# Optimization experiments

Hardware: AMD Instinct MI355X
Metric: run time of the kernel (lower is better)

Reference implementation:

```python
import jax, jax.numpy as jnp
import numpy as np

_SAMPLING_EPS = 1e-5


def setup_inputs() -> dict:
    key = jax.random.key(0)
    k1, k2, k3, k4, k5, k6 = jax.random.split(key, 6)
    B, V = 128, 128000
    return {
        "logits": jax.random.normal(k1, (B, V), dtype=jnp.float32),
        "temperature": jax.random.uniform(k2, (B,), dtype=jnp.float32),
        "min_p": jax.random.uniform(k3, (B,), dtype=jnp.float32),
        "top_k": jax.random.randint(k4, (B,), 0, 1024),
        "top_p": jax.random.uniform(k5, (B,), dtype=jnp.float32),
        "q": jax.random.uniform(k6, (B, V), dtype=jnp.float32),
        "num_logprobs": 20,
    }


def reference(logits, temperature, min_p, top_k, top_p, q, num_logprobs):
    B, V = logits.shape
    # raw logprobs computed BEFORE any processing (as in Sampler.forward)
    raw_logprobs = jax.nn.log_softmax(logits, axis=-1)
    # greedy sample on unscaled logits
    greedy = jnp.argmax(logits, axis=-1)
    # temperature scaling
    lt = logits / temperature[:, None]
    # min-p filtering
    probs = jax.nn.softmax(lt, axis=-1)
    max_p = jnp.max(probs, axis=-1, keepdims=True)
    lt = jnp.where(probs >= min_p[:, None] * max_p, lt, -jnp.inf)
    # top-k / top-p filtering on ascending-sorted logits (vLLM style)
    idx = jnp.argsort(lt, axis=-1)                       # ascending
    ls = jnp.take_along_axis(lt, idx, axis=-1)
    k = jnp.clip(top_k, 1, V)
    kth = jnp.take_along_axis(ls, (V - k)[:, None], axis=-1)  # k-th largest value
    ls = jnp.where(ls < kth, -jnp.inf, ls)
    ps = jax.nn.softmax(ls, axis=-1)
    csum = jnp.cumsum(ps, axis=-1)
    pmask = csum <= (1.0 - top_p)[:, None]
    pmask = pmask.at[:, -1].set(False)                   # always keep the max token
    ls = jnp.where(pmask, -jnp.inf, ls)
    inv = jnp.argsort(idx, axis=-1)                      # inverse permutation (scatter back)
    filtered = jnp.take_along_axis(ls, inv, axis=-1)
    # exponential-race sampling: argmax(probs / Exp(1)) ~ Categorical(probs)
    probs2 = jax.nn.softmax(filtered, axis=-1)
    expo = -jnp.log(jnp.clip(q, 1e-10, 1.0))
    rand_sampled = jnp.argmax(probs2 / expo, axis=-1)
    sampled = jnp.where(temperature < _SAMPLING_EPS, greedy, rand_sampled)
    # gather_logprobs: top-k logprobs + sampled-token logprob + rank
    topk_lp, topk_idx = jax.lax.top_k(raw_logprobs, num_logprobs)
    tok_lp = jnp.take_along_axis(raw_logprobs, sampled[:, None], axis=-1)  # (B,1)
    ranks = jnp.sum(raw_logprobs >= tok_lp, axis=-1)
    out_idx = jnp.concatenate([sampled[:, None], topk_idx], axis=1).astype(jnp.int32)
    out_lp = jnp.concatenate([tok_lp, topk_lp], axis=1)  # (B, num_logprobs+1)
    return (sampled[:, None].astype(jnp.int32), out_idx, out_lp, ranks)
```

## Files before the change

### kernel.cpp

```cpp
#include <hip/hip_runtime.h>
#include <math.h>

#define S_CHUNKS 16
#define NB 1024
#define C_CAP 2048
#define BLKA 256
#define BLK2 512
#define LCAP 1024
#define LCAP2 512
#define FLOORB 682
#define BIN_SCALE ((float)NB / 12.0f)

__device__ __forceinline__ int bin_of(float x) {
  int b = (int)floorf((x + 6.0f) * BIN_SCALE);
  return min(max(b, 0), NB - 1);
}
__device__ __forceinline__ unsigned long long pack_vi(float v, int idx) {
  return ((unsigned long long)__float_as_uint(v) << 32) | (unsigned int)idx;
}
__device__ __forceinline__ unsigned long long okey(float v, int idx) {
  unsigned int u = __float_as_uint(v);
  u = (u & 0x80000000u) ? ~u : (u | 0x80000000u);
  return ((unsigned long long)u << 32) | (unsigned long long)(0x7fffffffu - (unsigned int)idx);
}
__device__ __forceinline__ float okey_val(unsigned long long k) {
  unsigned int hi = (unsigned int)(k >> 32);
  unsigned int u = (hi & 0x80000000u) ? (hi & 0x7fffffffu) : ~hi;
  return __uint_as_float(u);
}
__device__ __forceinline__ int okey_idx(unsigned long long k) {
  return (int)(0x7fffffffu - (unsigned int)k);
}

__global__ __launch_bounds__(BLKA)
void kA_hist(const float* __restrict__ logits, int V, int chunkElems,
             unsigned short* __restrict__ chist, float* __restrict__ psum,
             unsigned long long* __restrict__ plist, int* __restrict__ pcnt) {
  const int row = blockIdx.y, chunk = blockIdx.x, tid = threadIdx.x;
  const float* lrow = logits + (size_t)row * V;
  const int start = chunk * chunkElems;
  const int end = min(start + chunkElems, V);
  __shared__ unsigned int hist[NB];
  __shared__ unsigned long long lst[LCAP2];
  __shared__ float rs[BLKA];
  __shared__ int lcnt;
  for (int i = tid; i < NB; i += BLKA) hist[i] = 0u;
  if (tid == 0) lcnt = 0;
  __syncthreads();
  float sum = 0.0f;
  const int n = max(end - start, 0);
  const int n4 = n >> 2;
  const float4* p4 = (const float4*)(lrow + start);
  for (int i = tid; i < n4; i += BLKA) {
    float4 a = p4[i];
    float va[4] = {a.x, a.y, a.z, a.w};
    #pragma unroll
    for (int c = 0; c < 4; c++) {
      float x = va[c];
      int b = bin_of(x);
      atomicAdd(&hist[b], 1u);
      sum += __expf(fminf(x, 70.0f) - 6.0f);
      if (b >= FLOORB) {
        int p = atomicAdd(&lcnt, 1);
        if (p < LCAP2) lst[p] = pack_vi(x, start + (i << 2) + c);
      }
    }
  }
  for (int j = (n4 << 2) + tid; j < n; j += BLKA) {
    float x = lrow[start + j];
    int b = bin_of(x);
    atomicAdd(&hist[b], 1u);
    sum += __expf(fminf(x, 70.0f) - 6.0f);
    if (b >= FLOORB) {
      int p = atomicAdd(&lcnt, 1);
      if (p < LCAP2) lst[p] = pack_vi(x, start + j);
    }
  }
  __syncthreads();
  rs[tid] = sum;
  __syncthreads();
  for (int s = BLKA / 2; s > 0; s >>= 1) {
    if (tid < s) rs[tid] += rs[tid + s];
    __syncthreads();
  }
  const size_t rc = (size_t)row * S_CHUNKS + chunk;
  if (tid == 0) { psum[rc] = rs[0]; pcnt[rc] = lcnt; }
  unsigned short* hrow = chist + rc * NB;
  for (int j = tid; j < NB; j += BLKA)
    hrow[j] = (unsigned short)min(hist[j], 65535u);
  int m = min(lcnt, LCAP2);
  unsigned long long* prow = plist + rc * LCAP2;
  for (int j = tid; j < m; j += BLKA) prow[j] = lst[j];
}

__global__ __launch_bounds__(BLKA)
void kB_select(const unsigned short* __restrict__ chist,
               const float* __restrict__ psum, const int* __restrict__ pcnt,
               const int* __restrict__ top_k, const int* __restrict__ nl_ptr,
               int V, int* __restrict__ bstar_out, float* __restrict__ lse_out,
               int* __restrict__ cnt, int* __restrict__ mode) {
  const int row = blockIdx.x, tid = threadIdx.x;
  __shared__ unsigned int h[NB];
  __shared__ int s_b, s_m;
  for (int i = tid; i < NB; i += BLKA) {
    unsigned int s = 0;
    for (int c = 0; c < S_CHUNKS; c++)
      s += chist[((size_t)row * S_CHUNKS + c) * NB + i];
    h[i] = s;
  }
  if (tid == 0) { s_b = 0; s_m = 0; }
  __syncthreads();
  if (tid < S_CHUNKS) atomicMax(&s_m, pcnt[(size_t)row * S_CHUNKS + tid]);
  for (int off = 1; off < NB; off <<= 1) {
    unsigned int t0[NB / BLKA];
    #pragma unroll
    for (int k = 0; k < NB / BLKA; k++) {
      int i = tid + k * BLKA;
      t0[k] = (i + off < NB) ? h[i + off] : 0u;
    }
    __syncthreads();
    #pragma unroll
    for (int k = 0; k < NB / BLKA; k++) h[tid + k * BLKA] += t0[k];
    __syncthreads();
  }
  int ke = top_k[row]; ke = min(max(ke, 1), V);
  int Kp = max(ke, nl_ptr[0]);
  #pragma unroll
  for (int k = 0; k < NB / BLKA; k++) {
    int i = tid + k * BLKA;
    if ((int)h[i] >= Kp) atomicMax(&s_b, i);
  }
  __syncthreads();
  if (tid == 0) {
    bstar_out[row] = s_b;
    float t = 0.0f;
    for (int c = 0; c < S_CHUNKS; c++) t += psum[(size_t)row * S_CHUNKS + c];
    lse_out[row] = 6.0f + logf(t);
    cnt[row] = 0;
    mode[row] = (s_b >= FLOORB && s_m <= LCAP2) ? 1 : 0;
  }
}

__global__ __launch_bounds__(BLKA)
void kC_collect(const float* __restrict__ logits, int V, int chunkElems,
                const int* __restrict__ bstar_in, const int* __restrict__ mode,
                const unsigned long long* __restrict__ plist,
                const int* __restrict__ pcnt, int* __restrict__ cnt,
                float* __restrict__ cand_val, int* __restrict__ cand_idx) {
  const int row = blockIdx.y, chunk = blockIdx.x, tid = threadIdx.x;
  const int bstar = bstar_in[row];
  __shared__ float lv[LCAP];
  __shared__ int   li[LCAP];
  __shared__ int   lcnt, gbase;
  if (tid == 0) lcnt = 0;
  __syncthreads();
  const size_t rc = (size_t)row * S_CHUNKS + chunk;
  if (mode[row]) {
    int m = min(pcnt[rc], LCAP2);
    const unsigned long long* prow = plist + rc * LCAP2;
    for (int j = tid; j < m; j += BLKA) {
      unsigned long long k = prow[j];
      float x = __uint_as_float((unsigned int)(k >> 32));
      int idx = (int)(unsigned int)k;
      if (bin_of(x) >= bstar) {
        int p = atomicAdd(&lcnt, 1);
        if (p < LCAP) { lv[p] = x; li[p] = idx; }
      }
    }
  } else {
    const float* lrow = logits + (size_t)row * V;
    const int start = chunk * chunkElems;
    const int end = min(start + chunkElems, V);
    const int n = max(end - start, 0);
    const int n4 = n >> 2;
    const float4* p4 = (const float4*)(lrow + start);
    for (int i = tid; i < n4; i += BLKA) {
      float4 a = p4[i];
      float va[4] = {a.x, a.y, a.z, a.w};
      #pragma unroll
      for (int c = 0; c < 4; c++) {
        if (bin_of(va[c]) >= bstar) {
          int p = atomicAdd(&lcnt, 1);
          if (p < LCAP) { lv[p] = va[c]; li[p] = start + (i << 2) + c; }
        }
      }
    }
    for (int j = (n4 << 2) + tid; j < n; j += BLKA) {
      float x = lrow[start + j];
      if (bin_of(x) >= bstar) {
        int p = atomicAdd(&lcnt, 1);
        if (p < LCAP) { lv[p] = x; li[p] = start + j; }
      }
    }
  }
  __syncthreads();
  int m = min(lcnt, LCAP);
  if (tid == 0) gbase = atomicAdd(&cnt[row], m);
  __syncthreads();
  int gb = gbase;
  for (int j = tid; j < m; j += BLKA) {
    int pos = gb + j;
    if (pos < C_CAP) {
      cand_val[(size_t)row * C_CAP + pos] = lv[j];
      cand_idx[(size_t)row * C_CAP + pos] = li[j];
    }
  }
}

__global__ __launch_bounds__(BLK2)
void k2_sample(const float* __restrict__ temperature,
               const float* __restrict__ min_p,
               const int* __restrict__ top_k,
               const float* __restrict__ top_p,
               const float* __restrict__ q,
               const int* __restrict__ nl_ptr,
               int V, int B,
               const float* __restrict__ cand_val,
               const int* __restrict__ cand_idx,
               const int* __restrict__ cnt_in,
               const float* __restrict__ lse_in,
               float* __restrict__ out) {
  const int row = blockIdx.x, tid = threadIdx.x;
  __shared__ int   scan[NB + 1];
  __shared__ unsigned long long bkt[C_CAP];
  __shared__ float sv[C_CAP];
  __shared__ int   si[C_CAP];
  __shared__ float ss[C_CAP];
  __shared__ float st[BLK2], rf[BLK2], rf2[BLK2];
  __shared__ int   ri[BLK2];
  __shared__ int   s_fail;

  int c = cnt_in[row]; c = min(c, C_CAP); c = max(c, 1);

  for (int i = tid; i <= NB; i += BLK2) scan[i] = 0;
  __syncthreads();

  unsigned long long mykey[4];
  int mybin[4], mya[4], myn = 0;
  #pragma unroll
  for (int r = 0; r < 4; r++) {
    int i = tid + r * BLK2;
    if (i < c) {
      float v = cand_val[(size_t)row * C_CAP + i];
      int id = cand_idx[(size_t)row * C_CAP + i];
      mykey[myn] = okey(v, id);
      int b = bin_of(v);
      mybin[myn] = b;
      mya[myn] = atomicAdd(&scan[b], 1);
      myn++;
    }
  }
  __syncthreads();
  for (int off = 1; off < NB; off <<= 1) {
    int i0 = tid, i1 = tid + BLK2;
    int t0 = (i0 + off < NB) ? scan[i0 + off] : 0;
    int t1 = (i1 + off < NB) ? scan[i1 + off] : 0;
    __syncthreads();
    scan[i0] += t0; scan[i1] += t1;
    __syncthreads();
  }
  for (int r = 0; r < myn; r++)
    bkt[scan[mybin[r] + 1] + mya[r]] = mykey[r];
  __syncthreads();
  for (int r = 0; r < myn; r++) {
    int gs = scan[mybin[r] + 1], ge = scan[mybin[r]];
    unsigned long long k0 = mykey[r];
    int rk = 0;
    for (int j = gs; j < ge; j++) if (bkt[j] > k0) rk++;
    int pos = gs + rk;
    sv[pos] = okey_val(k0);
    si[pos] = okey_idx(k0);
  }
  __syncthreads();

  float temp = temperature[row];
  bool ug = (temp < 1e-5f);
  float rt = 1.0f / (ug ? 1.0f : temp);
  float mp = min_p[row], tp = top_p[row];
  int nl = nl_ptr[0];
  int ke = top_k[row]; ke = min(max(ke, 1), V); ke = min(ke, c);
  float v0 = sv[0];
  float lt0 = v0 * rt;

  float ltk = sv[ke - 1] * rt;
  float kth = (expf(ltk - lt0) >= mp) ? ltk : -INFINITY;

  if (tid == 0) s_fail = c;
  __syncthreads();
  for (int i = tid; i < c; i += BLK2) {
    float ltj = sv[i] * rt;
    if (!((expf(ltj - lt0) >= mp) && (ltj >= kth))) { atomicMin(&s_fail, i); break; }
  }
  __syncthreads();
  int n1 = s_fail; if (n1 < 1) n1 = 1;
  __syncthreads();

  int L = (c + BLK2 - 1) / BLK2;
  int base = tid * L;
  int lim = min(base + L, c);
  float run = 0.0f;
  for (int j = base; j < lim; j++) {
    float pj = (j < n1) ? expf(sv[j] * rt - lt0) : 0.0f;
    run += pj; ss[j] = run;
  }
  st[tid] = run;
  __syncthreads();
  for (int off = 1; off < BLK2; off <<= 1) {
    float t0 = (tid >= off) ? st[tid - off] : 0.0f;
    __syncthreads();
    st[tid] += t0;
    __syncthreads();
  }
  float offv = (tid > 0) ? st[tid - 1] : 0.0f;
  for (int j = base; j < lim; j++) ss[j] += offv;
  __syncthreads();
  float Z1 = ss[n1 - 1];

  if (tid == 0) s_fail = n1;
  __syncthreads();
  for (int i = tid; i < n1; i += BLK2) {
    if (i > 0 && !((1.0f - ss[i - 1] / Z1) > (1.0f - tp))) { atomicMin(&s_fail, i); break; }
  }
  __syncthreads();
  int n2 = s_fail; if (n2 < 1) n2 = 1;
  __syncthreads();
  float Z2 = ss[n2 - 1];

  const float* qrow = q + (size_t)row * V;
  float bsc = -INFINITY; int bidx = 0x7fffffff; float bval = 0.0f;
  for (int i = tid; i < n2; i += BLK2) {
    float pj = expf(sv[i] * rt - lt0);
    float qv = qrow[si[i]];
    qv = fminf(fmaxf(qv, 1e-10f), 1.0f);
    float sc = (pj / Z2) / (-logf(qv));
    if (sc > bsc || (sc == bsc && si[i] < bidx)) { bsc = sc; bidx = si[i]; bval = sv[i]; }
  }
  rf[tid] = bsc; ri[tid] = bidx; rf2[tid] = bval;
  __syncthreads();
  for (int s = BLK2 / 2; s > 0; s >>= 1) {
    if (tid < s) {
      if (rf[tid + s] > rf[tid] ||
          (rf[tid + s] == rf[tid] && ri[tid + s] < ri[tid])) {
        rf[tid] = rf[tid + s]; ri[tid] = ri[tid + s]; rf2[tid] = rf2[tid + s];
      }
    }
    __syncthreads();
  }
  int sampled = ug ? si[0] : ri[0];
  float val_s = ug ? sv[0] : rf2[0];
  float lse = lse_in[row];
  float tok_lp = val_s - lse;
  __syncthreads();

  if (tid == 0) s_fail = c;
  __syncthreads();
  for (int i = tid; i < c; i += BLK2)
    if (!((sv[i] - lse) >= tok_lp)) { atomicMin(&s_fail, i); break; }
  __syncthreads();
  int rank = s_fail;

  int W = nl + 1;
  if (tid == 0) {
    out[row] = (float)sampled;
    out[B + row * W] = (float)sampled;
    out[B + B * W + row * W] = tok_lp;
    out[B + 2 * B * W + row] = (float)rank;
  }
  for (int t = tid; t < nl; t += BLK2) {
    out[B + row * W + 1 + t] = (float)si[t];
    out[B + B * W + row * W + 1 + t] = sv[t] - lse;
  }
}

extern "C" void kernel_launch(void* const* d_in, const int* in_sizes, int n_in,
                              void* d_out, int out_size, void* d_ws, size_t ws_size,
                              hipStream_t stream) {
  const float* logits      = (const float*)d_in[0];
  const float* temperature = (const float*)d_in[1];
  const float* min_p       = (const float*)d_in[2];
  const int*   top_k       = (const int*)d_in[3];
  const float* top_p       = (const float*)d_in[4];
  const float* q           = (const float*)d_in[5];
  const int*   nl_ptr      = (const int*)d_in[6];

  int B = in_sizes[1];
  int V = in_sizes[0] / B;
  float* out = (float*)d_out;
  int chunkElems = ((V + S_CHUNKS - 1) / S_CHUNKS + 3) & ~3;

  unsigned char* w = (unsigned char*)d_ws;
  unsigned long long* plist = (unsigned long long*)w; w += (size_t)B * S_CHUNKS * LCAP2 * sizeof(unsigned long long);
  unsigned short* chist = (unsigned short*)w;         w += (size_t)B * S_CHUNKS * NB * sizeof(unsigned short);
  float* psum = (float*)w;                            w += (size_t)B * S_CHUNKS * sizeof(float);
  int* pcnt = (int*)w;                                w += (size_t)B * S_CHUNKS * sizeof(int);
  int* bstar = (int*)w;                               w += (size_t)B * sizeof(int);
  float* lse = (float*)w;                             w += (size_t)B * sizeof(float);
  int* cnt = (int*)w;                                 w += (size_t)B * sizeof(int);
  int* mode = (int*)w;                                w += (size_t)B * sizeof(int);
  float* cand_val = (float*)w;                        w += (size_t)B * C_CAP * sizeof(float);
  int* cand_idx = (int*)w;                            w += (size_t)B * C_CAP * sizeof(int);

  hipLaunchKernelGGL(kA_hist, dim3(S_CHUNKS, B), dim3(BLKA), 0, stream,
                     logits, V, chunkElems, chist, psum, plist, pcnt);
  hipLaunchKernelGGL(kB_select, dim3(B), dim3(BLKA), 0, stream,
                     chist, psum, pcnt, top_k, nl_ptr, V, bstar, lse, cnt, mode);
  hipLaunchKernelGGL(kC_collect, dim3(S_CHUNKS, B), dim3(BLKA), 0, stream,
                     logits, V, chunkElems, bstar, mode, plist, pcnt, cnt,
                     cand_val, cand_idx);
  hipLaunchKernelGGL(k2_sample, dim3(B), dim3(BLK2), 0, stream,
                     temperature, min_p, top_k, top_p, q, nl_ptr, V, B,
                     cand_val, cand_idx, cnt, lse, out);
}
```

Before: 185.8 us.

## Fuse bin selection, candidate collection and sampling into one per-row kernel

Merges the select, collect and sample kernels into a single per-row block. The block sums the chunk histograms, finds the threshold bin, scatters candidates straight into shared-memory bucket slots using the histogram prefix offsets, and then samples. This removes two kernel launches and the global candidate buffers. The fallback path now scans the whole row with only one block per row instead of sixteen. The histogram pass also processes two float4 loads per iteration to raise memory-level parallelism.

```diff
diff --git a/kernel.cpp b/kernel.cpp
--- a/kernel.cpp
+++ b/kernel.cpp
@@ -6,7 +6,6 @@
 #define C_CAP 2048
 #define BLKA 256
 #define BLK2 512
-#define LCAP 1024
 #define LCAP2 512
 #define FLOORB 682
 #define BIN_SCALE ((float)NB / 12.0f)
@@ -51,7 +50,26 @@
   const int n = max(end - start, 0);
   const int n4 = n >> 2;
   const float4* p4 = (const float4*)(lrow + start);
-  for (int i = tid; i < n4; i += BLKA) {
+  int i = tid;
+  for (; i + BLKA < n4; i += 2 * BLKA) {
+    float4 a = p4[i], b2 = p4[i + BLKA];
+    float va[8] = {a.x, a.y, a.z, a.w, b2.x, b2.y, b2.z, b2.w};
+    int ia[8];
+    #pragma unroll
+    for (int c = 0; c < 4; c++) { ia[c] = start + (i << 2) + c; ia[c + 4] = start + ((i + BLKA) << 2) + c; }
+    #pragma unroll
+    for (int c = 0; c < 8; c++) {
+      float x = va[c];
+      int b = bin_of(x);
+      atomicAdd(&hist[b], 1u);
+      sum += __expf(fminf(x, 70.0f) - 6.0f);
+      if (b >= FLOORB) {
+        int p = atomicAdd(&lcnt, 1);
+        if (p < LCAP2) lst[p] = pack_vi(x, ia[c]);
+      }
+    }
+  }
+  for (; i < n4; i += BLKA) {
     float4 a = p4[i];
     float va[4] = {a.x, a.y, a.z, a.w};
     #pragma unroll
@@ -93,183 +111,129 @@
   for (int j = tid; j < m; j += BLKA) prow[j] = lst[j];
 }
 
-__global__ __launch_bounds__(BLKA)
-void kB_select(const unsigned short* __restrict__ chist,
-               const float* __restrict__ psum, const int* __restrict__ pcnt,
-               const int* __restrict__ top_k, const int* __restrict__ nl_ptr,
-               int V, int* __restrict__ bstar_out, float* __restrict__ lse_out,
-               int* __restrict__ cnt, int* __restrict__ mode) {
+__global__ __launch_bounds__(BLK2)
+void k2_fused(const float* __restrict__ logits,
+              const float* __restrict__ temperature,
+              const float* __restrict__ min_p,
+              const int* __restrict__ top_k,
+              const float* __restrict__ top_p,
+              const float* __restrict__ q,
+              const int* __restrict__ nl_ptr,
+              int V, int B, int chunkElems,
+              const unsigned short* __restrict__ chist,
+              const float* __restrict__ psum,
+              const unsigned long long* __restrict__ plist,
+              const int* __restrict__ pcnt,
+              float* __restrict__ out) {
   const int row = blockIdx.x, tid = threadIdx.x;
-  __shared__ unsigned int h[NB];
-  __shared__ int s_b, s_m;
-  for (int i = tid; i < NB; i += BLKA) {
-    unsigned int s = 0;
-    for (int c = 0; c < S_CHUNKS; c++)
-      s += chist[((size_t)row * S_CHUNKS + c) * NB + i];
-    h[i] = s;
-  }
-  if (tid == 0) { s_b = 0; s_m = 0; }
-  __syncthreads();
-  if (tid < S_CHUNKS) atomicMax(&s_m, pcnt[(size_t)row * S_CHUNKS + tid]);
-  for (int off = 1; off < NB; off <<= 1) {
-    unsigned int t0[NB / BLKA];
-    #pragma unroll
-    for (int k = 0; k < NB / BLKA; k++) {
-      int i = tid + k * BLKA;
-      t0[k] = (i + off < NB) ? h[i + off] : 0u;
-    }
-    __syncthreads();
-    #pragma unroll
-    for (int k = 0; k < NB / BLKA; k++) h[tid + k * BLKA] += t0[k];
-    __syncthreads();
-  }
-  int ke = top_k[row]; ke = min(max(ke, 1), V);
-  int Kp = max(ke, nl_ptr[0]);
-  #pragma unroll
-  for (int k = 0; k < NB / BLKA; k++) {
-    int i = tid + k * BLKA;
-    if ((int)h[i] >= Kp) atomicMax(&s_b, i);
-  }
-  __syncthreads();
-  if (tid == 0) {
-    bstar_out[row] = s_b;
-    float t = 0.0f;
-    for (int c = 0; c < S_CHUNKS; c++) t += psum[(size_t)row * S_CHUNKS + c];
-    lse_out[row] = 6.0f + logf(t);
-    cnt[row] = 0;
-    mode[row] = (s_b >= FLOORB && s_m <= LCAP2) ? 1 : 0;
-  }
-}
-
-__global__ __launch_bounds__(BLKA)
-void kC_collect(const float* __restrict__ logits, int V, int chunkElems,
-                const int* __restrict__ bstar_in, const int* __restrict__ mode,
-                const unsigned long long* __restrict__ plist,
-                const int* __restrict__ pcnt, int* __restrict__ cnt,
-                float* __restrict__ cand_val, int* __restrict__ cand_idx) {
-  const int row = blockIdx.y, chunk = blockIdx.x, tid = threadIdx.x;
-  const int bstar = bstar_in[row];
-  __shared__ float lv[LCAP];
-  __shared__ int   li[LCAP];
-  __shared__ int   lcnt, gbase;
-  if (tid == 0) lcnt = 0;
-  __syncthreads();
-  const size_t rc = (size_t)row * S_CHUNKS + chunk;
-  if (mode[row]) {
-    int m = min(pcnt[rc], LCAP2);
-    const unsigned long long* prow = plist + rc * LCAP2;
-    for (int j = tid; j < m; j += BLKA) {
-      unsigned long long k = prow[j];
-      float x = __uint_as_float((unsigned int)(k >> 32));
-      int idx = (int)(unsigned int)k;
-      if (bin_of(x) >= bstar) {
-        int p = atomicAdd(&lcnt, 1);
-        if (p < LCAP) { lv[p] = x; li[p] = idx; }
-      }
-    }
-  } else {
-    const float* lrow = logits + (size_t)row * V;
-    const int start = chunk * chunkElems;
-    const int end = min(start + chunkElems, V);
-    const int n = max(end - start, 0);
-    const int n4 = n >> 2;
-    const float4* p4 = (const float4*)(lrow + start);
-    for (int i = tid; i < n4; i += BLKA) {
-      float4 a = p4[i];
-      float va[4] = {a.x, a.y, a.z, a.w};
-      #pragma unroll
-      for (int c = 0; c < 4; c++) {
-        if (bin_of(va[c]) >= bstar) {
-          int p = atomicAdd(&lcnt, 1);
-          if (p < LCAP) { lv[p] = va[c]; li[p] = start + (i << 2) + c; }
-        }
-      }
-    }
-    for (int j = (n4 << 2) + tid; j < n; j += BLKA) {
-      float x = lrow[start + j];
-      if (bin_of(x) >= bstar) {
-        int p = atomicAdd(&lcnt, 1);
-        if (p < LCAP) { lv[p] = x; li[p] = start + j; }
-      }
-    }
-  }
-  __syncthreads();
-  int m = min(lcnt, LCAP);
-  if (tid == 0) gbase = atomicAdd(&cnt[row], m);
-  __syncthreads();
-  int gb = gbase;
-  for (int j = tid; j < m; j += BLKA) {
-    int pos = gb + j;
-    if (pos < C_CAP) {
-      cand_val[(size_t)row * C_CAP + pos] = lv[j];
-      cand_idx[(size_t)row * C_CAP + pos] = li[j];
-    }
-  }
-}
-
-__global__ __launch_bounds__(BLK2)
-void k2_sample(const float* __restrict__ temperature,
-               const float* __restrict__ min_p,
-               const int* __restrict__ top_k,
-               const float* __restrict__ top_p,
-               const float* __restrict__ q,
-               const int* __restrict__ nl_ptr,
-               int V, int B,
-               const float* __restrict__ cand_val,
-               const int* __restrict__ cand_idx,
-               const int* __restrict__ cnt_in,
-               const float* __restrict__ lse_in,
-               float* __restrict__ out) {
-  const int row = blockIdx.x, tid = threadIdx.x;
-  __shared__ int   scan[NB + 1];
+  __shared__ int h[NB + 1];
+  __shared__ int cur[NB];
   __shared__ unsigned long long bkt[C_CAP];
   __shared__ float sv[C_CAP];
   __shared__ int   si[C_CAP];
   __shared__ float ss[C_CAP];
   __shared__ float st[BLK2], rf[BLK2], rf2[BLK2];
   __shared__ int   ri[BLK2];
-  __shared__ int   s_fail;
-
-  int c = cnt_in[row]; c = min(c, C_CAP); c = max(c, 1);
-
-  for (int i = tid; i <= NB; i += BLK2) scan[i] = 0;
-  __syncthreads();
-
-  unsigned long long mykey[4];
-  int mybin[4], mya[4], myn = 0;
+  __shared__ int   s_fail, s_b, s_m;
+  __shared__ float s_lse;
+
   #pragma unroll
-  for (int r = 0; r < 4; r++) {
-    int i = tid + r * BLK2;
-    if (i < c) {
-      float v = cand_val[(size_t)row * C_CAP + i];
-      int id = cand_idx[(size_t)row * C_CAP + i];
-      mykey[myn] = okey(v, id);
-      int b = bin_of(v);
-      mybin[myn] = b;
-      mya[myn] = atomicAdd(&scan[b], 1);
-      myn++;
-    }
-  }
-  __syncthreads();
+  for (int k = 0; k < NB / BLK2; k++) {
+    int i = tid + k * BLK2;
+    int s = 0;
+    for (int c = 0; c < S_CHUNKS; c++)
+      s += chist[((size_t)row * S_CHUNKS + c) * NB + i];
+    h[i] = s;
+    cur[i] = 0;
+  }
+  if (tid == 0) { h[NB] = 0; s_b = 0; s_m = 0; s_fail = 0; }
+  __syncthreads();
+  if (tid < S_CHUNKS) atomicMax(&s_m, pcnt[(size_t)row * S_CHUNKS + tid]);
   for (int off = 1; off < NB; off <<= 1) {
-    int i0 = tid, i1 = tid + BLK2;
-    int t0 = (i0 + off < NB) ? scan[i0 + off] : 0;
-    int t1 = (i1 + off < NB) ? scan[i1 + off] : 0;
-    __syncthreads();
-    scan[i0] += t0; scan[i1] += t1;
-    __syncthreads();
-  }
-  for (int r = 0; r < myn; r++)
-    bkt[scan[mybin[r] + 1] + mya[r]] = mykey[r];
-  __syncthreads();
-  for (int r = 0; r < myn; r++) {
-    int gs = scan[mybin[r] + 1], ge = scan[mybin[r]];
-    unsigned long long k0 = mykey[r];
+    int t0[NB / BLK2];
+    #pragma unroll
+    for (int k = 0; k < NB / BLK2; k++) {
+      int i = tid + k * BLK2;
+      t0[k] = (i + off < NB) ? h[i + off] : 0;
+    }
+    __syncthreads();
+    #pragma unroll
+    for (int k = 0; k < NB / BLK2; k++) h[tid + k * BLK2] += t0[k];
+    __syncthreads();
+  }
+  int nl = nl_ptr[0];
+  int ke = top_k[row]; ke = min(max(ke, 1), V);
+  int Kp = max(ke, nl);
+  #pragma unroll
+  for (int k = 0; k < NB / BLK2; k++) {
+    int i = tid + k * BLK2;
+    if (h[i] >= Kp) atomicMax(&s_b, i);
+  }
+  if (tid == 0) {
+    float t = 0.0f;
+    for (int c = 0; c < S_CHUNKS; c++) t += psum[(size_t)row * S_CHUNKS + c];
+    s_lse = 6.0f + logf(t);
+  }
+  __syncthreads();
+  const int bstar = s_b;
+  const bool fast = (bstar >= FLOORB && s_m <= LCAP2);
+  int c = min(h[bstar], C_CAP); if (c < 1) c = 1;
+
+  if (fast) {
+    for (int chunk = 0; chunk < S_CHUNKS; chunk++) {
+      const size_t rc = (size_t)row * S_CHUNKS + chunk;
+      const int m = pcnt[rc];
+      const unsigned long long* prow = plist + rc * LCAP2;
+      for (int j = tid; j < m; j += BLK2) {
+        unsigned long long kk = prow[j];
+        float x = __uint_as_float((unsigned int)(kk >> 32));
+        int idx = (int)(unsigned int)kk;
+        int b = bin_of(x);
+        if (b >= bstar) {
+          int a = atomicAdd(&cur[b], 1);
+          int pos = h[b + 1] + a;
+          if (pos < C_CAP) bkt[pos] = okey(x, idx);
+        }
+      }
+    }
+  } else {
+    const float* lrow = logits + (size_t)row * V;
+    const int n4 = V >> 2;
+    const float4* p4 = (const float4*)lrow;
+    for (int i = tid; i < n4; i += BLK2) {
+      float4 a4 = p4[i];
+      float va[4] = {a4.x, a4.y, a4.z, a4.w};
+      #pragma unroll
+      for (int cc = 0; cc < 4; cc++) {
+        int b = bin_of(va[cc]);
+        if (b >= bstar) {
+          int a = atomicAdd(&cur[b], 1);
+          int pos = h[b + 1] + a;
+          if (pos < C_CAP) bkt[pos] = okey(va[cc], (i << 2) + cc);
+        }
+      }
+    }
+    for (int j = (n4 << 2) + tid; j < V; j += BLK2) {
+      float x = lrow[j];
+      int b = bin_of(x);
+      if (b >= bstar) {
+        int a = atomicAdd(&cur[b], 1);
+        int pos = h[b + 1] + a;
+        if (pos < C_CAP) bkt[pos] = okey(x, j);
+      }
+    }
+  }
+  __syncthreads();
+  for (int pos = tid; pos < c; pos += BLK2) {
+    unsigned long long k0 = bkt[pos];
+    float v = okey_val(k0);
+    int b = bin_of(v);
+    int gs = h[b + 1];
+    int ge = min(h[b], c);
     int rk = 0;
     for (int j = gs; j < ge; j++) if (bkt[j] > k0) rk++;
-    int pos = gs + rk;
-    sv[pos] = okey_val(k0);
-    si[pos] = okey_idx(k0);
+    int fin = gs + rk;
+    sv[fin] = v; si[fin] = okey_idx(k0);
   }
   __syncthreads();
 
@@ -277,8 +241,7 @@
   bool ug = (temp < 1e-5f);
   float rt = 1.0f / (ug ? 1.0f : temp);
   float mp = min_p[row], tp = top_p[row];
-  int nl = nl_ptr[0];
-  int ke = top_k[row]; ke = min(max(ke, 1), V); ke = min(ke, c);
+  ke = min(ke, c);
   float v0 = sv[0];
   float lt0 = v0 * rt;
 
@@ -348,7 +311,7 @@
   }
   int sampled = ug ? si[0] : ri[0];
   float val_s = ug ? sv[0] : rf2[0];
-  float lse = lse_in[row];
+  float lse = s_lse;
   float tok_lp = val_s - lse;
   __syncthreads();
 
@@ -393,21 +356,10 @@
   unsigned short* chist = (unsigned short*)w;         w += (size_t)B * S_CHUNKS * NB * sizeof(unsigned short);
   float* psum = (float*)w;                            w += (size_t)B * S_CHUNKS * sizeof(float);
   int* pcnt = (int*)w;                                w += (size_t)B * S_CHUNKS * sizeof(int);
-  int* bstar = (int*)w;                               w += (size_t)B * sizeof(int);
-  float* lse = (float*)w;                             w += (size_t)B * sizeof(float);
-  int* cnt = (int*)w;                                 w += (size_t)B * sizeof(int);
-  int* mode = (int*)w;                                w += (size_t)B * sizeof(int);
-  float* cand_val = (float*)w;                        w += (size_t)B * C_CAP * sizeof(float);
-  int* cand_idx = (int*)w;                            w += (size_t)B * C_CAP * sizeof(int);
 
   hipLaunchKernelGGL(kA_hist, dim3(S_CHUNKS, B), dim3(BLKA), 0, stream,
                      logits, V, chunkElems, chist, psum, plist, pcnt);
-  hipLaunchKernelGGL(kB_select, dim3(B), dim3(BLKA), 0, stream,
-                     chist, psum, pcnt, top_k, nl_ptr, V, bstar, lse, cnt, mode);
-  hipLaunchKernelGGL(kC_collect, dim3(S_CHUNKS, B), dim3(BLKA), 0, stream,
-                     logits, V, chunkElems, bstar, mode, plist, pcnt, cnt,
-                     cand_val, cand_idx);
-  hipLaunchKernelGGL(k2_sample, dim3(B), dim3(BLK2), 0, stream,
-                     temperature, min_p, top_k, top_p, q, nl_ptr, V, B,
-                     cand_val, cand_idx, cnt, lse, out);
-}
+  hipLaunchKernelGGL(k2_fused, dim3(B), dim3(BLK2), 0, stream,
+                     logits, temperature, min_p, top_k, top_p, q, nl_ptr,
+                     V, B, chunkElems, chist, psum, plist, pcnt, out);
+}
```

New measurement: 175.6 us. 1.06x faster.
